# Optimization experiments

Measured on AMD Instinct MI355X. Metric: run time of the kernel, lower is better.

The kernel has to match this reference:

```python
import jax, jax.numpy as jnp
import numpy as np

ALPHA = 1.5      # entmax alpha (q parameter)
N_ITER = 50      # entmax-bisect iterations (entmax library default)
B, S, DM, H, HKV, HD = 1, 2048, 2048, 16, 4, 128
ROPE_THETA = 10000.0


def _entmax_p(x):
    """alpha-entmax along last axis via bisection on tau (matches entmax.EntmaxBisect)."""
    am1 = ALPHA - 1.0
    pw = 1.0 / am1
    X = x * am1
    d = x.shape[-1]
    max_val = jnp.max(X, axis=-1, keepdims=True)
    tau_lo = max_val - 1.0                      # _gp(1, alpha) = 1
    tau_hi = max_val - (1.0 / d) ** am1          # _gp(1/d, alpha)
    dm0 = tau_hi - tau_lo

    def body(i, carry):
        tau_lo, dm, tau_m = carry
        dm = dm * 0.5
        tau_m = tau_lo + dm
        p = jnp.maximum(X - tau_m, 0.0) ** pw
        f = jnp.sum(p, axis=-1, keepdims=True) - 1.0
        tau_lo = jnp.where(f >= 0, tau_m, tau_lo)
        return (tau_lo, dm, tau_m)

    tau_lo, dm, tau_m = jax.lax.fori_loop(0, N_ITER, body, (tau_lo, dm0, tau_lo))
    p = jnp.maximum(X - tau_m, 0.0) ** pw
    return p / jnp.sum(p, axis=-1, keepdims=True)  # ensure_sum_one


@jax.custom_vjp
def entmax_bisect(x):
    return _entmax_p(x)

def _emx_fwd(x):
    p = _entmax_p(x)
    return p, p

def _emx_bwd(p, g):
    # entmax library backward: gppr = p^(2-alpha) on support
    gppr = jnp.where(p > 0, p ** (2.0 - ALPHA), 0.0)
    dX = g * gppr
    q = jnp.sum(dX, axis=-1, keepdims=True) / jnp.sum(gppr, axis=-1, keepdims=True)
    return ((dX - q * gppr),)

entmax_bisect.defvjp(_emx_fwd, _emx_bwd)


def _rotate_half(x):
    x1, x2 = x[..., : HD // 2], x[..., HD // 2:]
    return jnp.concatenate([-x2, x1], axis=-1)


def setup_inputs() -> dict:
    key = jax.random.key(0)
    k1, k2, k3, k4, k5 = jax.random.split(key, 5)
    hidden_states = jax.random.normal(k1, (B, S, DM), dtype=jnp.float32)
    wq = jax.random.normal(k2, (H * HD, DM), dtype=jnp.float32) * 0.02
    wk = jax.random.normal(k3, (HKV * HD, DM), dtype=jnp.float32) * 0.02
    wv = jax.random.normal(k4, (HKV * HD, DM), dtype=jnp.float32) * 0.02
    wo = jax.random.normal(k5, (DM, H * HD), dtype=jnp.float32) * 0.02
    # real Llama RoPE position embeddings
    inv_freq = 1.0 / (ROPE_THETA ** (np.arange(0, HD, 2, dtype=np.float32) / HD))
    pos = np.arange(S, dtype=np.float32)
    freqs = pos[:, None] * inv_freq[None, :]          # [S, HD/2]
    emb = np.concatenate([freqs, freqs], axis=-1)     # [S, HD]
    cos = jnp.asarray(np.cos(emb))[None]              # [1, S, HD]
    sin = jnp.asarray(np.sin(emb))[None]
    return {"hidden_states": hidden_states, "cos": cos, "sin": sin,
            "wq": wq, "wk": wk, "wv": wv, "wo": wo}


def reference(hidden_states, cos, sin, wq, wk, wv, wo):
    b, s, _ = hidden_states.shape
    scaling = HD ** -0.5
    # QKV projections -> [B, H, S, HD]
    q = (hidden_states @ wq.T).reshape(b, s, H, HD).transpose(0, 2, 1, 3)
    k = (hidden_states @ wk.T).reshape(b, s, HKV, HD).transpose(0, 2, 1, 3)
    v = (hidden_states @ wv.T).reshape(b, s, HKV, HD).transpose(0, 2, 1, 3)
    # RoPE (cos/sin broadcast over head axis)
    c, sn = cos[:, None, :, :], sin[:, None, :, :]
    q = q * c + _rotate_half(q) * sn
    k = k * c + _rotate_half(k) * sn
    # GQA: repeat kv heads
    g = H // HKV
    k = jnp.repeat(k, g, axis=1)
    v = jnp.repeat(v, g, axis=1)
    scores = jnp.einsum('bhqd,bhkd->bhqk', q, k) * scaling
    causal = jnp.tril(jnp.ones((s, s), dtype=bool))
    scores = jnp.where(causal, scores, -jnp.inf)
    attn = entmax_bisect(scores)                      # [B, H, S, S]
    out = jnp.einsum('bhqk,bhkd->bhqd', attn, v)
    out = out.transpose(0, 2, 1, 3).reshape(b, s, H * HD)
    out = out @ wo.T
    return (out, attn)
```

## Files before the change

### kernel.cpp

```cpp
#include <hip/hip_runtime.h>

typedef __bf16 bf16;
typedef __bf16 bf16x4 __attribute__((ext_vector_type(4)));
typedef __bf16 bf16x8 __attribute__((ext_vector_type(8)));
typedef float f32x4 __attribute__((ext_vector_type(4)));
typedef float f32x2 __attribute__((ext_vector_type(2)));

#define S 2048
#define DM 2048
#define HD 128
#define H 16
#define NQKV 3072
#define AS_ITERS 3
#define NW_ITERS 3
#define BROW 556

__device__ __forceinline__ void gl2lds16(const void* g, void* l) {
    __builtin_amdgcn_global_load_lds(
        (const __attribute__((address_space(1))) void*)g,
        (__attribute__((address_space(3))) void*)l, 16, 0, 0);
}

__device__ __forceinline__ void nt_store4(f32x4 v, float* p) {
    __builtin_nontemporal_store(v, (f32x4*)p);
}

template <int CTRL, int RM>
__device__ __forceinline__ float dpp_zero(float x) {
    return __builtin_bit_cast(float, __builtin_amdgcn_update_dpp(
        0, __builtin_bit_cast(int, x), CTRL, RM, 0xf, false));
}
template <int CTRL, int RM>
__device__ __forceinline__ float dpp_self(float x) {
    int xi = __builtin_bit_cast(int, x);
    return __builtin_bit_cast(float, __builtin_amdgcn_update_dpp(xi, xi, CTRL, RM, 0xf, false));
}
__device__ __forceinline__ float wave_bcast63(float x) {
    return __builtin_bit_cast(float, __builtin_amdgcn_readlane(__builtin_bit_cast(int, x), 63));
}
__device__ __forceinline__ float wave_sum(float x) {
    x += dpp_zero<0x111, 0xf>(x);
    x += dpp_zero<0x112, 0xf>(x);
    x += dpp_zero<0x114, 0xf>(x);
    x += dpp_zero<0x118, 0xf>(x);
    x += dpp_zero<0x142, 0xa>(x);
    x += dpp_zero<0x143, 0xc>(x);
    return wave_bcast63(x);
}
__device__ __forceinline__ float wave_fmax(float x) {
    x = fmaxf(x, dpp_self<0x111, 0xf>(x));
    x = fmaxf(x, dpp_self<0x112, 0xf>(x));
    x = fmaxf(x, dpp_self<0x114, 0xf>(x));
    x = fmaxf(x, dpp_self<0x118, 0xf>(x));
    x = fmaxf(x, dpp_self<0x142, 0xa>(x));
    x = fmaxf(x, dpp_self<0x143, 0xc>(x));
    return wave_bcast63(x);
}

__global__ void cvt_all(const float* __restrict__ hid, const float* __restrict__ wq,
                        const float* __restrict__ wk, const float* __restrict__ wv,
                        const float* __restrict__ wo, bf16* __restrict__ bh,
                        bf16* __restrict__ bqkv, bf16* __restrict__ bwo) {
    int i = blockIdx.x * blockDim.x + threadIdx.x;
    const float* src;
    bf16* dst;
    int off;
    if (i < 1048576) { src = hid; dst = bh; off = i; }
    else if (i < 2097152) { src = wq; dst = bqkv; off = i - 1048576; }
    else if (i < 2359296) { src = wk; dst = bqkv + 2048 * 2048; off = i - 2097152; }
    else if (i < 2621440) { src = wv; dst = bqkv + 2048 * 2048 + 512 * 2048; off = i - 2359296; }
    else { src = wo; dst = bwo; off = i - 2621440; }
    float4 f = ((const float4*)src)[off];
    bf16x4 o;
    o[0] = (bf16)f.x; o[1] = (bf16)f.y; o[2] = (bf16)f.z; o[3] = (bf16)f.w;
    ((bf16x4*)dst)[off] = o;
}

__global__ __launch_bounds__(256) void gemm_qkv_rope(const bf16* __restrict__ A,
                                                     const bf16* __restrict__ B,
                                                     const float* __restrict__ cosb,
                                                     const float* __restrict__ sinb,
                                                     bf16* __restrict__ qs,
                                                     bf16* __restrict__ kb,
                                                     bf16* __restrict__ vT) {
    constexpr int BM = 64, BN = 128, K = DM;
    __shared__ bf16 As[2][BM * 32];
    __shared__ bf16 Bs[2][BN * 32];
    __shared__ float ct[32][129];
    int m0 = blockIdx.x * BM;
    int by = blockIdx.y;
    int n0 = by * BN;
    int t = threadIdx.x;
    int l = t & 63, w = t >> 6;
    int lane16 = l & 15, quad = l >> 4;

    const bf16* Abase = A + (size_t)m0 * K;
    const bf16* Bbase = B + (size_t)n0 * K;

    constexpr int MI = BM / 32, NI = BN / 32;
    int wm = (w & 1) * (BM / 2), wn = (w >> 1) * (BN / 2);
    f32x4 acc[MI][NI];
#pragma unroll
    for (int i = 0; i < MI; i++)
#pragma unroll
        for (int j = 0; j < NI; j++) acc[i][j] = (f32x4){0.f, 0.f, 0.f, 0.f};

    constexpr int AG = BM * 4;
    constexpr int BG = BN * 4;

    auto stage = [&](int sel, int k0) {
#pragma unroll
        for (int it = 0; it < AG / 256; it++) {
            int c = it * 256 + t;
            gl2lds16(Abase + (size_t)(c >> 2) * K + k0 + (c & 3) * 8, &As[sel][(c - l) * 8]);
        }
#pragma unroll
        for (int it = 0; it < BG / 256; it++) {
            int c = it * 256 + t;
            gl2lds16(Bbase + (size_t)(c >> 2) * K + k0 + (c & 3) * 8, &Bs[sel][(c - l) * 8]);
        }
    };

    stage(0, 0);
    __syncthreads();
    int cur = 0;
    for (int k0 = 0; k0 < K; k0 += 32) {
        if (k0 + 32 < K) stage(cur ^ 1, k0 + 32);
        bf16x8 af[MI], bfr[NI];
#pragma unroll
        for (int i = 0; i < MI; i++)
            af[i] = *(const bf16x8*)&As[cur][(wm + i * 16 + lane16) * 32 + quad * 8];
#pragma unroll
        for (int j = 0; j < NI; j++)
            bfr[j] = *(const bf16x8*)&Bs[cur][(wn + j * 16 + lane16) * 32 + quad * 8];
#pragma unroll
        for (int i = 0; i < MI; i++)
#pragma unroll
            for (int j = 0; j < NI; j++)
                acc[i][j] = __builtin_amdgcn_mfma_f32_16x16x32_bf16(af[i], bfr[j], acc[i][j], 0, 0, 0);
        __syncthreads();
        cur ^= 1;
    }

#pragma unroll
    for (int half = 0; half < 2; half++) {
        if ((w & 1) == half) {
#pragma unroll
            for (int i = 0; i < MI; i++)
#pragma unroll
                for (int j = 0; j < NI; j++)
#pragma unroll
                    for (int r = 0; r < 4; r++)
                        ct[i * 16 + quad * 4 + r][wn + j * 16 + lane16] = acc[i][j][r];
        }
        __syncthreads();
        if (by < 20) {
#pragma unroll
            for (int it = 0; it < 16; it++) {
                int idx = it * 256 + t;
                int row = idx >> 7, d = idx & 127;
                int s = m0 + half * 32 + row;
                float v = ct[row][d];
                float other = ct[row][(d < 64) ? (d + 64) : (d - 64)];
                float c = cosb[s * HD + d], sn = sinb[s * HD + d];
                float rot = (d < 64) ? -other : other;
                float o = v * c + rot * sn;
                if (by < 16)
                    qs[((size_t)by * S + s) * HD + d] = (bf16)(o * 0.04419417382415922f);
                else
                    kb[((size_t)(by - 16) * S + s) * HD + d] = (bf16)o;
            }
        } else {
            int y0 = (by - 20) * 128;
#pragma unroll
            for (int it = 0; it < 16; it++) {
                int idx = it * 256 + t;
                int y = idx >> 5, ss = idx & 31;
                vT[(size_t)(y0 + y) * S + m0 + half * 32 + ss] = (bf16)ct[ss][y];
            }
        }
        __syncthreads();
    }
}

template <int BM, int BN>
__global__ __launch_bounds__(256) void gemm_bt(const bf16* __restrict__ A,
                                               const bf16* __restrict__ B,
                                               float* __restrict__ C, int Ndim, int K) {
    __shared__ bf16 As[2][BM * 32];
    __shared__ bf16 Bs[2][BN * 32];
    int m0 = blockIdx.x * BM, n0 = blockIdx.y * BN;
    int t = threadIdx.x;
    int l = t & 63, w = t >> 6;
    int lane16 = l & 15, quad = l >> 4;

    const bf16* Abase = A + (size_t)m0 * K;
    const bf16* Bbase = B + (size_t)n0 * K;

    constexpr int MI = BM / 32, NI = BN / 32;
    int wm = (w & 1) * (BM / 2), wn = (w >> 1) * (BN / 2);
    f32x4 acc[MI][NI];
#pragma unroll
    for (int i = 0; i < MI; i++)
#pragma unroll
        for (int j = 0; j < NI; j++) acc[i][j] = (f32x4){0.f, 0.f, 0.f, 0.f};

    constexpr int AG = BM * 4;
    constexpr int BG = BN * 4;

    auto stage = [&](int sel, int k0) {
#pragma unroll
        for (int it = 0; it < AG / 256; it++) {
            int c = it * 256 + t;
            gl2lds16(Abase + (size_t)(c >> 2) * K + k0 + (c & 3) * 8, &As[sel][(c - l) * 8]);
        }
#pragma unroll
        for (int it = 0; it < BG / 256; it++) {
            int c = it * 256 + t;
            gl2lds16(Bbase + (size_t)(c >> 2) * K + k0 + (c & 3) * 8, &Bs[sel][(c - l) * 8]);
        }
    };

    stage(0, 0);
    __syncthreads();
    int cur = 0;
    for (int k0 = 0; k0 < K; k0 += 32) {
        if (k0 + 32 < K) stage(cur ^ 1, k0 + 32);
        bf16x8 af[MI], bfr[NI];
#pragma unroll
        for (int i = 0; i < MI; i++)
            af[i] = *(const bf16x8*)&As[cur][(wm + i * 16 + lane16) * 32 + quad * 8];
#pragma unroll
        for (int j = 0; j < NI; j++)
            bfr[j] = *(const bf16x8*)&Bs[cur][(wn + j * 16 + lane16) * 32 + quad * 8];
#pragma unroll
        for (int i = 0; i < MI; i++)
#pragma unroll
            for (int j = 0; j < NI; j++)
                acc[i][j] = __builtin_amdgcn_mfma_f32_16x16x32_bf16(af[i], bfr[j], acc[i][j], 0, 0, 0);
        __syncthreads();
        cur ^= 1;
    }
#pragma unroll
    for (int i = 0; i < MI; i++)
#pragma unroll
        for (int j = 0; j < NI; j++) {
            float* cp = C + (size_t)(m0 + wm + i * 16 + quad * 4) * Ndim + n0 + wn + j * 16 + lane16;
#pragma unroll
            for (int r = 0; r < 4; r++) cp[(size_t)r * Ndim] = acc[i][j][r];
        }
}

template <int SEGS>
__device__ __forceinline__ void attn_body(const bf16* __restrict__ qs, const bf16* __restrict__ kb,
                                          const bf16* __restrict__ vT, float* __restrict__ attn,
                                          bf16* __restrict__ o, int r0, int h,
                                          float (&buf)[16][BROW]) {
    constexpr int NREG2 = SEGS * 4;
    int jlen = r0 + 16;
    int l = threadIdx.x & 63;
    int w = threadIdx.x >> 6;
    int lane16 = l & 15, quad = l >> 4;

    const bf16* qrow = qs + ((size_t)h * S + (r0 + lane16)) * HD + quad * 8;
    bf16x8 afrag[4];
#pragma unroll
    for (int kc = 0; kc < 4; kc++) afrag[kc] = *(const bf16x8*)(qrow + kc * 32);

    const bf16* kbase = kb + (size_t)(h >> 2) * S * HD;
    const bf16* vbase = vT + (size_t)(h >> 2) * HD * S;
    f32x2 xr[NREG2];

#pragma unroll
    for (int sgi = 0; sgi < SEGS; sgi++) {
        int j0 = sgi * 512;
#pragma unroll
        for (int tt = 0; tt < 2; tt++) {
            int t = w + tt * 16;
            int jt = j0 + t * 16;
            if (jt < jlen) {
                f32x4 acc = {0.f, 0.f, 0.f, 0.f};
                const bf16* kp = kbase + (size_t)(jt + lane16) * HD + quad * 8;
#pragma unroll
                for (int kc = 0; kc < 4; kc++) {
                    bf16x8 b = *(const bf16x8*)(kp + kc * 32);
                    acc = __builtin_amdgcn_mfma_f32_16x16x32_bf16(afrag[kc], b, acc, 0, 0, 0);
                }
                if (jt + 15 > r0) {
                    int jj = jt + lane16;
#pragma unroll
                    for (int r = 0; r < 4; r++) {
                        int rowi = quad * 4 + r;
                        float v = acc[r];
                        if (jj > r0 + rowi) v = -1e30f;
                        buf[rowi][t * 16 + lane16] = v;
                    }
                } else {
#pragma unroll
                    for (int r = 0; r < 4; r++) buf[quad * 4 + r][t * 16 + lane16] = acc[r];
                }
            }
        }
        __syncthreads();
#pragma unroll
        for (int part = 0; part < 2; part++) {
            float4 fq = *(const float4*)&buf[w][part * 256 + l * 4];
            if (sgi == SEGS - 1) {
                int jb = j0 + part * 256 + l * 4;
                xr[sgi * 4 + part * 2 + 0] =
                    (f32x2){(jb + 0 < jlen) ? fq.x : -1e30f, (jb + 1 < jlen) ? fq.y : -1e30f};
                xr[sgi * 4 + part * 2 + 1] =
                    (f32x2){(jb + 2 < jlen) ? fq.z : -1e30f, (jb + 3 < jlen) ? fq.w : -1e30f};
            } else {
                xr[sgi * 4 + part * 2 + 0] = (f32x2){fq.x, fq.y};
                xr[sgi * 4 + part * 2 + 1] = (f32x2){fq.z, fq.w};
            }
        }
        __syncthreads();
    }

    float* arow = attn + ((size_t)h * S + (r0 + w)) * S;

    {
        f32x4 z4 = {0.f, 0.f, 0.f, 0.f};
        for (int j = SEGS * 512 + l * 4; j < S; j += 256) nt_store4(z4, &arow[j]);
    }

    const f32x2 z2 = {0.f, 0.f};
    float mx = -1e30f;
#pragma unroll
    for (int c = 0; c < NREG2; c++) mx = fmaxf(mx, fmaxf(xr[c][0], xr[c][1]));
    float m = wave_fmax(mx);
    float taulo = m - 1.0f;
    float tauhi = m - 0.02209709f;
    float tau = taulo;

#pragma unroll 1
    for (int it = 0; it < AS_ITERS; it++) {
        f32x2 tvi = {tau, tau};
        f32x2 b1a = z2, b1b = z2, b2a = z2, b2b = z2, cna = z2, cnb = z2;
#pragma unroll
        for (int c = 0; c < NREG2; c += 2) {
            f32x2 t0 = __builtin_elementwise_max(xr[c] - tvi, z2);
            b2a += t0 * t0; b1a += t0;
            cna += (f32x2){t0[0] > 0.f ? 1.f : 0.f, t0[1] > 0.f ? 1.f : 0.f};
            f32x2 t1 = __builtin_elementwise_max(xr[c + 1] - tvi, z2);
            b2b += t1 * t1; b1b += t1;
            cnb += (f32x2){t1[0] > 0.f ? 1.f : 0.f, t1[1] > 0.f ? 1.f : 0.f};
        }
        f32x2 s1 = b1a + b1b, s2 = b2a + b2b, sc = cna + cnb;
        float B1 = wave_sum(s1[0] + s1[1]);
        float B2 = wave_sum(s2[0] + s2[1]);
        float n = wave_sum(sc[0] + sc[1]);
        float disc = fmaxf(B1 * B1 - n * (B2 - 1.0f), 0.f);
        tau += (B1 - __builtin_sqrtf(disc)) / fmaxf(n, 1.0f);
        tau = fminf(fmaxf(tau, taulo), tauhi);
    }
#pragma unroll 1
    for (int it = 0; it < NW_ITERS; it++) {
        f32x2 tvi = {tau, tau};
        f32x2 fa = z2, fb = z2, ga = z2, gb = z2;
#pragma unroll
        for (int c = 0; c < NREG2; c += 2) {
            f32x2 t0 = __builtin_elementwise_max(xr[c] - tvi, z2);
            fa += t0 * t0; ga += t0;
            f32x2 t1 = __builtin_elementwise_max(xr[c + 1] - tvi, z2);
            fb += t1 * t1; gb += t1;
        }
        f32x2 fv = fa + fb, gv = ga + gb;
        float f = wave_sum(fv[0] + fv[1]);
        float g = wave_sum(gv[0] + gv[1]);
        tau += (f - 1.0f) / (2.0f * g + 1e-20f);
        tau = fminf(fmaxf(tau, taulo), tauhi);
    }

    f32x2 tv = {tau, tau};
    float inv;
    {
        f32x2 sa = z2, sbv = z2;
#pragma unroll
        for (int c = 0; c < NREG2; c += 2) {
            f32x2 t0 = __builtin_elementwise_max(xr[c] - tv, z2);
            sa += t0 * t0;
            f32x2 t1 = __builtin_elementwise_max(xr[c + 1] - tv, z2);
            sbv += t1 * t1;
        }
        f32x2 sv = sa + sbv;
        float ssum = wave_sum(sv[0] + sv[1]);
        inv = 1.0f / ssum;
    }

    int jt_o = (w & 7) * 16;
    int kh = (w >> 3) * 256;
    f32x4 acc_o = {0.f, 0.f, 0.f, 0.f};
    f32x2 inv2 = {inv, inv};

#pragma unroll
    for (int sgi = 0; sgi < SEGS; sgi++) {
        int j0 = sgi * 512;
        bf16 (*pb)[BROW] = (bf16(*)[BROW])(&buf[0][0]) + (sgi & 1) * 16;
#pragma unroll
        for (int part = 0; part < 2; part++) {
            f32x2 ta = __builtin_elementwise_max(xr[sgi * 4 + part * 2 + 0] - tv, z2);
            f32x2 tb = __builtin_elementwise_max(xr[sgi * 4 + part * 2 + 1] - tv, z2);
            f32x2 pa = (ta * ta) * inv2;
            f32x2 pb2 = (tb * tb) * inv2;
            f32x4 pv = {pa[0], pa[1], pb2[0], pb2[1]};
            nt_store4(pv, &arow[j0 + part * 256 + l * 4]);
            bf16x4 pbv;
            pbv[0] = (bf16)pv[0]; pbv[1] = (bf16)pv[1];
            pbv[2] = (bf16)pv[2]; pbv[3] = (bf16)pv[3];
            *(bf16x4*)&pb[w][part * 256 + l * 4] = pbv;
        }
        __syncthreads();
#pragma unroll
        for (int ks = 0; ks < 8; ks++) {
            int kk = kh + ks * 32;
            bf16x8 a = *(const bf16x8*)&pb[lane16][kk + quad * 8];
            bf16x8 b = *(const bf16x8*)(vbase + (size_t)(jt_o + lane16) * S + j0 + kk + quad * 8);
            acc_o = __builtin_amdgcn_mfma_f32_16x16x32_bf16(a, b, acc_o, 0, 0, 0);
        }
    }

    __syncthreads();
    if (w >= 8) {
#pragma unroll
        for (int r = 0; r < 4; r++) buf[w - 8][l * 4 + r] = acc_o[r];
    }
    __syncthreads();
    if (w < 8) {
        bf16* op = o + (size_t)(r0 + quad * 4) * DM + h * HD + jt_o + lane16;
#pragma unroll
        for (int r = 0; r < 4; r++) {
            float v = acc_o[r] + buf[w][l * 4 + r];
            op[(size_t)r * DM] = (bf16)v;
        }
    }
}

__global__ __launch_bounds__(1024, 8) void attn_av_all(const bf16* __restrict__ qs,
                                                       const bf16* __restrict__ kb,
                                                       const bf16* __restrict__ vT,
                                                       float* __restrict__ attn,
                                                       bf16* __restrict__ o) {
    __shared__ float buf[16][BROW];
    int b = blockIdx.x;
    int h = b & 15;
    int qh = b >> 4;
    attn_body<4>(qs, kb, vT, attn, o, (96 + qh) * 16, h, buf);
    __syncthreads();
    attn_body<3>(qs, kb, vT, attn, o, (64 + qh) * 16, h, buf);
    __syncthreads();
    attn_body<2>(qs, kb, vT, attn, o, (32 + qh) * 16, h, buf);
    __syncthreads();
    attn_body<1>(qs, kb, vT, attn, o, qh * 16, h, buf);
}

extern "C" void kernel_launch(void* const* d_in, const int* in_sizes, int n_in,
                              void* d_out, int out_size, void* d_ws, size_t ws_size,
                              hipStream_t stream) {
    const float* hidden = (const float*)d_in[0];
    const float* cosb   = (const float*)d_in[1];
    const float* sinb   = (const float*)d_in[2];
    const float* wq     = (const float*)d_in[3];
    const float* wk     = (const float*)d_in[4];
    const float* wv     = (const float*)d_in[5];
    const float* wo     = (const float*)d_in[6];
    char* ws = (char*)d_ws;
    bf16*  bf_hidden = (bf16*)(ws);
    bf16*  bf_wqkv   = (bf16*)(ws + 8388608);
    bf16*  bf_wo     = (bf16*)(ws + 20971520);
    bf16*  qsb       = (bf16*)(ws + 29360128);
    bf16*  kbb       = (bf16*)(ws + 37748736);
    bf16*  vTb       = (bf16*)(ws + 39845888);
    float* out  = (float*)d_out;
    float* attn = out + 4194304;

    cvt_all<<<dim3(14336), 256, 0, stream>>>(hidden, wq, wk, wv, wo, bf_hidden, bf_wqkv, bf_wo);

    gemm_qkv_rope<<<dim3(32, 24), 256, 0, stream>>>(bf_hidden, bf_wqkv, cosb, sinb,
                                                    qsb, kbb, vTb);

    attn_av_all<<<dim3(512), 1024, 0, stream>>>(qsb, kbb, vTb, attn, bf_hidden);

    gemm_bt<64, 128><<<dim3(32, 16), 256, 0, stream>>>(bf_hidden, bf_wo, out, DM, DM);
}
```

Before: 567.1 us.

## Keep fp16 score rows in shared memory instead of fp32 register arrays

Scores are now written as fp16 into one full-row LDS buffer (16 x 2056 halves) instead of being staged segment by segment in fp32 LDS and held in per-lane register arrays. Each root-finding iteration re-reads its row from LDS, and the probability row is written in bf16 over the same buffer before a single P·V pass. This removes the per-segment barriers and the large register footprint, which should raise occupancy. In exchange it adds LDS read traffic on every iteration and rounds the scores to fp16 (mask value -30000), which costs precision.

```diff
diff --git a/kernel.cpp b/kernel.cpp
--- a/kernel.cpp
+++ b/kernel.cpp
@@ -5,6 +5,7 @@
 typedef __bf16 bf16x8 __attribute__((ext_vector_type(8)));
 typedef float f32x4 __attribute__((ext_vector_type(4)));
 typedef float f32x2 __attribute__((ext_vector_type(2)));
+typedef _Float16 f16x8 __attribute__((ext_vector_type(8)));
 
 #define S 2048
 #define DM 2048
@@ -13,7 +14,8 @@
 #define NQKV 3072
 #define AS_ITERS 3
 #define NW_ITERS 3
-#define BROW 556
+#define SROW 2056
+#define MASKV -30000.0f
 
 __device__ __forceinline__ void gl2lds16(const void* g, void* l) {
     __builtin_amdgcn_global_load_lds(
@@ -255,11 +257,11 @@
 __device__ __forceinline__ void attn_body(const bf16* __restrict__ qs, const bf16* __restrict__ kb,
                                           const bf16* __restrict__ vT, float* __restrict__ attn,
                                           bf16* __restrict__ o, int r0, int h,
-                                          float (&buf)[16][BROW]) {
-    constexpr int NREG2 = SEGS * 4;
+                                          _Float16 (&sb)[16][SROW]) {
     int jlen = r0 + 16;
-    int l = threadIdx.x & 63;
-    int w = threadIdx.x >> 6;
+    int t = threadIdx.x;
+    int l = t & 63;
+    int w = t >> 6;
     int lane16 = l & 15, quad = l >> 4;
 
     const bf16* qrow = qs + ((size_t)h * S + (r0 + lane16)) * HD + quad * 8;
@@ -269,15 +271,21 @@
 
     const bf16* kbase = kb + (size_t)(h >> 2) * S * HD;
     const bf16* vbase = vT + (size_t)(h >> 2) * HD * S;
-    f32x2 xr[NREG2];
+
+    {
+        f16x8 mk = {(_Float16)MASKV, (_Float16)MASKV, (_Float16)MASKV, (_Float16)MASKV,
+                    (_Float16)MASKV, (_Float16)MASKV, (_Float16)MASKV, (_Float16)MASKV};
+        int row = t >> 6;
+        for (int c = jlen + (t & 63) * 8; c < SEGS * 512; c += 512)
+            *(f16x8*)&sb[row][c] = mk;
+    }
 
 #pragma unroll
     for (int sgi = 0; sgi < SEGS; sgi++) {
         int j0 = sgi * 512;
 #pragma unroll
         for (int tt = 0; tt < 2; tt++) {
-            int t = w + tt * 16;
-            int jt = j0 + t * 16;
+            int jt = j0 + (w + tt * 16) * 16;
             if (jt < jlen) {
                 f32x4 acc = {0.f, 0.f, 0.f, 0.f};
                 const bf16* kp = kbase + (size_t)(jt + lane16) * HD + quad * 8;
@@ -290,34 +298,19 @@
                     int jj = jt + lane16;
 #pragma unroll
                     for (int r = 0; r < 4; r++) {
-                        int rowi = quad * 4 + r;
                         float v = acc[r];
-                        if (jj > r0 + rowi) v = -1e30f;
-                        buf[rowi][t * 16 + lane16] = v;
+                        if (jj > r0 + quad * 4 + r) v = MASKV;
+                        sb[quad * 4 + r][jt + lane16] = (_Float16)v;
                     }
                 } else {
 #pragma unroll
-                    for (int r = 0; r < 4; r++) buf[quad * 4 + r][t * 16 + lane16] = acc[r];
+                    for (int r = 0; r < 4; r++)
+                        sb[quad * 4 + r][jt + lane16] = (_Float16)acc[r];
                 }
             }
         }
-        __syncthreads();
-#pragma unroll
-        for (int part = 0; part < 2; part++) {
-            float4 fq = *(const float4*)&buf[w][part * 256 + l * 4];
-            if (sgi == SEGS - 1) {
-                int jb = j0 + part * 256 + l * 4;
-                xr[sgi * 4 + part * 2 + 0] =
-                    (f32x2){(jb + 0 < jlen) ? fq.x : -1e30f, (jb + 1 < jlen) ? fq.y : -1e30f};
-                xr[sgi * 4 + part * 2 + 1] =
-                    (f32x2){(jb + 2 < jlen) ? fq.z : -1e30f, (jb + 3 < jlen) ? fq.w : -1e30f};
-            } else {
-                xr[sgi * 4 + part * 2 + 0] = (f32x2){fq.x, fq.y};
-                xr[sgi * 4 + part * 2 + 1] = (f32x2){fq.z, fq.w};
-            }
-        }
-        __syncthreads();
-    }
+    }
+    __syncthreads();
 
     float* arow = attn + ((size_t)h * S + (r0 + w)) * S;
 
@@ -326,10 +319,14 @@
         for (int j = SEGS * 512 + l * 4; j < S; j += 256) nt_store4(z4, &arow[j]);
     }
 
-    const f32x2 z2 = {0.f, 0.f};
-    float mx = -1e30f;
-#pragma unroll
-    for (int c = 0; c < NREG2; c++) mx = fmaxf(mx, fmaxf(xr[c][0], xr[c][1]));
+    const _Float16* myrow = &sb[w][0];
+    float mx = MASKV;
+#pragma unroll
+    for (int j = 0; j < SEGS; j++) {
+        f16x8 v = *(const f16x8*)&myrow[j * 512 + l * 8];
+#pragma unroll
+        for (int e = 0; e < 8; e++) mx = fmaxf(mx, (float)v[e]);
+    }
     float m = wave_fmax(mx);
     float taulo = m - 1.0f;
     float tauhi = m - 0.02209709f;
@@ -337,102 +334,108 @@
 
 #pragma unroll 1
     for (int it = 0; it < AS_ITERS; it++) {
-        f32x2 tvi = {tau, tau};
-        f32x2 b1a = z2, b1b = z2, b2a = z2, b2b = z2, cna = z2, cnb = z2;
-#pragma unroll
-        for (int c = 0; c < NREG2; c += 2) {
-            f32x2 t0 = __builtin_elementwise_max(xr[c] - tvi, z2);
-            b2a += t0 * t0; b1a += t0;
-            cna += (f32x2){t0[0] > 0.f ? 1.f : 0.f, t0[1] > 0.f ? 1.f : 0.f};
-            f32x2 t1 = __builtin_elementwise_max(xr[c + 1] - tvi, z2);
-            b2b += t1 * t1; b1b += t1;
-            cnb += (f32x2){t1[0] > 0.f ? 1.f : 0.f, t1[1] > 0.f ? 1.f : 0.f};
-        }
-        f32x2 s1 = b1a + b1b, s2 = b2a + b2b, sc = cna + cnb;
-        float B1 = wave_sum(s1[0] + s1[1]);
-        float B2 = wave_sum(s2[0] + s2[1]);
-        float n = wave_sum(sc[0] + sc[1]);
+        float b1 = 0.f, b2 = 0.f, cn = 0.f;
+#pragma unroll
+        for (int j = 0; j < SEGS; j++) {
+            f16x8 v = *(const f16x8*)&myrow[j * 512 + l * 8];
+#pragma unroll
+            for (int e = 0; e < 8; e++) {
+                float d = fmaxf((float)v[e] - tau, 0.f);
+                b2 = fmaf(d, d, b2);
+                b1 += d;
+                cn += (d > 0.f) ? 1.f : 0.f;
+            }
+        }
+        float B1 = wave_sum(b1);
+        float B2 = wave_sum(b2);
+        float n = wave_sum(cn);
         float disc = fmaxf(B1 * B1 - n * (B2 - 1.0f), 0.f);
         tau += (B1 - __builtin_sqrtf(disc)) / fmaxf(n, 1.0f);
         tau = fminf(fmaxf(tau, taulo), tauhi);
     }
 #pragma unroll 1
     for (int it = 0; it < NW_ITERS; it++) {
-        f32x2 tvi = {tau, tau};
-        f32x2 fa = z2, fb = z2, ga = z2, gb = z2;
-#pragma unroll
-        for (int c = 0; c < NREG2; c += 2) {
-            f32x2 t0 = __builtin_elementwise_max(xr[c] - tvi, z2);
-            fa += t0 * t0; ga += t0;
-            f32x2 t1 = __builtin_elementwise_max(xr[c + 1] - tvi, z2);
-            fb += t1 * t1; gb += t1;
-        }
-        f32x2 fv = fa + fb, gv = ga + gb;
-        float f = wave_sum(fv[0] + fv[1]);
-        float g = wave_sum(gv[0] + gv[1]);
-        tau += (f - 1.0f) / (2.0f * g + 1e-20f);
+        float f = 0.f, g = 0.f;
+#pragma unroll
+        for (int j = 0; j < SEGS; j++) {
+            f16x8 v = *(const f16x8*)&myrow[j * 512 + l * 8];
+#pragma unroll
+            for (int e = 0; e < 8; e++) {
+                float d = fmaxf((float)v[e] - tau, 0.f);
+                f = fmaf(d, d, f);
+                g += d;
+            }
+        }
+        float F = wave_sum(f);
+        float G = wave_sum(g);
+        tau += (F - 1.0f) / (2.0f * G + 1e-20f);
         tau = fminf(fmaxf(tau, taulo), tauhi);
     }
-
-    f32x2 tv = {tau, tau};
     float inv;
     {
-        f32x2 sa = z2, sbv = z2;
-#pragma unroll
-        for (int c = 0; c < NREG2; c += 2) {
-            f32x2 t0 = __builtin_elementwise_max(xr[c] - tv, z2);
-            sa += t0 * t0;
-            f32x2 t1 = __builtin_elementwise_max(xr[c + 1] - tv, z2);
-            sbv += t1 * t1;
-        }
-        f32x2 sv = sa + sbv;
-        float ssum = wave_sum(sv[0] + sv[1]);
-        inv = 1.0f / ssum;
-    }
-
+        float s = 0.f;
+#pragma unroll
+        for (int j = 0; j < SEGS; j++) {
+            f16x8 v = *(const f16x8*)&myrow[j * 512 + l * 8];
+#pragma unroll
+            for (int e = 0; e < 8; e++) {
+                float d = fmaxf((float)v[e] - tau, 0.f);
+                s = fmaf(d, d, s);
+            }
+        }
+        inv = 1.0f / wave_sum(s);
+    }
+
+    bf16* prow = (bf16*)&sb[0][0] + (size_t)w * SROW;
+#pragma unroll
+    for (int j = 0; j < SEGS; j++) {
+        int c = j * 512 + l * 8;
+        f16x8 v = *(const f16x8*)&myrow[c];
+        float p[8];
+#pragma unroll
+        for (int e = 0; e < 8; e++) {
+            float d = fmaxf((float)v[e] - tau, 0.f);
+            p[e] = d * d * inv;
+        }
+        f32x4 p0 = {p[0], p[1], p[2], p[3]};
+        f32x4 p1 = {p[4], p[5], p[6], p[7]};
+        nt_store4(p0, &arow[c]);
+        nt_store4(p1, &arow[c + 4]);
+        bf16x8 pb;
+#pragma unroll
+        for (int e = 0; e < 8; e++) pb[e] = (bf16)p[e];
+        *(bf16x8*)&prow[c] = pb;
+    }
+    __syncthreads();
+
+    const bf16* pbuf = (const bf16*)&sb[0][0];
     int jt_o = (w & 7) * 16;
     int kh = (w >> 3) * 256;
     f32x4 acc_o = {0.f, 0.f, 0.f, 0.f};
-    f32x2 inv2 = {inv, inv};
-
 #pragma unroll
     for (int sgi = 0; sgi < SEGS; sgi++) {
         int j0 = sgi * 512;
-        bf16 (*pb)[BROW] = (bf16(*)[BROW])(&buf[0][0]) + (sgi & 1) * 16;
-#pragma unroll
-        for (int part = 0; part < 2; part++) {
-            f32x2 ta = __builtin_elementwise_max(xr[sgi * 4 + part * 2 + 0] - tv, z2);
-            f32x2 tb = __builtin_elementwise_max(xr[sgi * 4 + part * 2 + 1] - tv, z2);
-            f32x2 pa = (ta * ta) * inv2;
-            f32x2 pb2 = (tb * tb) * inv2;
-            f32x4 pv = {pa[0], pa[1], pb2[0], pb2[1]};
-            nt_store4(pv, &arow[j0 + part * 256 + l * 4]);
-            bf16x4 pbv;
-            pbv[0] = (bf16)pv[0]; pbv[1] = (bf16)pv[1];
-            pbv[2] = (bf16)pv[2]; pbv[3] = (bf16)pv[3];
-            *(bf16x4*)&pb[w][part * 256 + l * 4] = pbv;
-        }
-        __syncthreads();
 #pragma unroll
         for (int ks = 0; ks < 8; ks++) {
             int kk = kh + ks * 32;
-            bf16x8 a = *(const bf16x8*)&pb[lane16][kk + quad * 8];
+            bf16x8 a = *(const bf16x8*)&pbuf[(size_t)lane16 * SROW + j0 + kk + quad * 8];
             bf16x8 b = *(const bf16x8*)(vbase + (size_t)(jt_o + lane16) * S + j0 + kk + quad * 8);
             acc_o = __builtin_amdgcn_mfma_f32_16x16x32_bf16(a, b, acc_o, 0, 0, 0);
         }
     }
 
     __syncthreads();
+    float* fs = (float*)&sb[0][0];
     if (w >= 8) {
 #pragma unroll
-        for (int r = 0; r < 4; r++) buf[w - 8][l * 4 + r] = acc_o[r];
+        for (int r = 0; r < 4; r++) fs[(w - 8) * 256 + l * 4 + r] = acc_o[r];
     }
     __syncthreads();
     if (w < 8) {
         bf16* op = o + (size_t)(r0 + quad * 4) * DM + h * HD + jt_o + lane16;
 #pragma unroll
         for (int r = 0; r < 4; r++) {
-            float v = acc_o[r] + buf[w][l * 4 + r];
+            float v = acc_o[r] + fs[w * 256 + l * 4 + r];
             op[(size_t)r * DM] = (bf16)v;
         }
     }
@@ -443,17 +446,17 @@
                                                        const bf16* __restrict__ vT,
                                                        float* __restrict__ attn,
                                                        bf16* __restrict__ o) {
-    __shared__ float buf[16][BROW];
+    __shared__ _Float16 sb[16][SROW];
     int b = blockIdx.x;
     int h = b & 15;
     int qh = b >> 4;
-    attn_body<4>(qs, kb, vT, attn, o, (96 + qh) * 16, h, buf);
-    __syncthreads();
-    attn_body<3>(qs, kb, vT, attn, o, (64 + qh) * 16, h, buf);
-    __syncthreads();
-    attn_body<2>(qs, kb, vT, attn, o, (32 + qh) * 16, h, buf);
-    __syncthreads();
-    attn_body<1>(qs, kb, vT, attn, o, qh * 16, h, buf);
+    attn_body<4>(qs, kb, vT, attn, o, (96 + qh) * 16, h, sb);
+    __syncthreads();
+    attn_body<3>(qs, kb, vT, attn, o, (64 + qh) * 16, h, sb);
+    __syncthreads();
+    attn_body<2>(qs, kb, vT, attn, o, (32 + qh) * 16, h, sb);
+    __syncthreads();
+    attn_body<1>(qs, kb, vT, attn, o, qh * 16, h, sb);
 }
 
 extern "C" void kernel_launch(void* const* d_in, const int* in_sizes, int n_in,
```

New measurement: 564.5 us. About the same (-0.5%).
